# Performance work log

Measured on AMD Instinct MI355X. Metric: run time of the kernel, lower is better.

The kernel has to match this reference:

```python
import jax, jax.numpy as jnp
import numpy as np

B, T, D, U = 32, 4096, 512, 512

def setup_inputs() -> dict:
    key = jax.random.key(0)
    ks = jax.random.split(key, 8)
    s = 0.02
    return {
        "query": jax.random.normal(ks[0], (B, D), dtype=jnp.float32),
        "values": jax.random.normal(ks[1], (B, T, D), dtype=jnp.float32),
        "W1": jax.random.normal(ks[2], (D, U), dtype=jnp.float32) * s,
        "b1": jnp.zeros((U,), dtype=jnp.float32),
        "W2": jax.random.normal(ks[3], (D, U), dtype=jnp.float32) * s,
        "b2": jnp.zeros((U,), dtype=jnp.float32),
        "V": jax.random.normal(ks[4], (U, 1), dtype=jnp.float32) * s,
        "bv": jnp.zeros((1,), dtype=jnp.float32),
    }

def reference(query, values, W1, b1, W2, b2, V, bv):
    # query: [B, D] -> [B, 1, U]; values: [B, T, D] -> [B, T, U]
    q_proj = (query @ W1 + b1)[:, None, :]            # [B, 1, U]
    v_proj = values @ W2 + b2                          # [B, T, U]
    scores = jnp.tanh(q_proj + v_proj) @ V + bv        # [B, T, 1]
    attn = jax.nn.softmax(scores, axis=1)              # softmax over time axis
    context = jnp.sum(attn * values, axis=1)           # [B, D]
    return context
```

## Files before the change

### kernel.cpp

```cpp
#include <hip/hip_runtime.h>
#include <hip/hip_bf16.h>
#include <math.h>

#define B_ 32
#define T_ 4096
#define D_ 512
#define U_ 512

typedef __bf16 bf16x8 __attribute__((ext_vector_type(8)));
typedef float floatx4 __attribute__((ext_vector_type(4)));
typedef unsigned short ushortx8 __attribute__((ext_vector_type(8)));

static __device__ __forceinline__ unsigned short f2bf(float f) {
  unsigned int u = __float_as_uint(f);
  unsigned int r = (u + 0x7fffu + ((u >> 16) & 1u)) >> 16;
  return (unsigned short)r;
}

__global__ __launch_bounds__(256) void prep_w2t(
    const float* __restrict__ W2, unsigned short* __restrict__ W2T) {
  __shared__ float tile[32][33];
  const int bx = blockIdx.x * 32;
  const int by = blockIdx.y * 32;
  const int x = threadIdx.x;
#pragma unroll
  for (int y = threadIdx.y; y < 32; y += 8)
    tile[y][x] = W2[(size_t)(bx + y) * U_ + by + x];
  __syncthreads();
#pragma unroll
  for (int y = threadIdx.y; y < 32; y += 8)
    W2T[(size_t)(by + y) * D_ + bx + x] = f2bf(tile[x][y]);
}

__global__ __launch_bounds__(256) void qproj_kernel(
    const float* __restrict__ query, const float* __restrict__ W1,
    const float* __restrict__ b1, const float* __restrict__ b2,
    float* __restrict__ qp) {
  const int b = blockIdx.x;
  const int tid = threadIdx.x;
  __shared__ float qs[D_];
  qs[tid] = query[b * D_ + tid];
  qs[tid + 256] = query[b * D_ + tid + 256];
  __syncthreads();
  const int u0 = tid * 2;
  float ax = 0.f, ay = 0.f;
#pragma unroll 8
  for (int k = 0; k < D_; ++k) {
    const float q = qs[k];
    const float2 w = *(const float2*)&W1[(size_t)k * U_ + u0];
    ax += q * w.x;
    ay += q * w.y;
  }
  qp[b * U_ + u0] = ax + b1[u0] + b2[u0];
  qp[b * U_ + u0 + 1] = ay + b1[u0 + 1] + b2[u0 + 1];
}

__global__ __launch_bounds__(256) void scores_mfma(
    const float* __restrict__ values, const unsigned short* __restrict__ W2T,
    const float* __restrict__ qp, const float* __restrict__ V,
    float* __restrict__ scores) {
  const int b = blockIdx.y;
  const int t0 = blockIdx.x * 128;
  const int u0 = blockIdx.z * 128;
  const int tid = threadIdx.x;

  __shared__ __align__(16) unsigned short As[128 * 32];
  __shared__ __align__(16) unsigned short Bs[128 * 32];

  const int w = tid >> 6;
  const int lane = tid & 63;
  const int mo = (w & 1) * 64;
  const int no = (w >> 1) * 64;
  const int lr = lane & 15;
  const int koff = (lane >> 4) * 8;

  const float* vbase = values + ((size_t)b * T_ + t0) * D_;

  floatx4 acc[4][4];
#pragma unroll
  for (int i = 0; i < 4; ++i)
#pragma unroll
    for (int j = 0; j < 4; ++j) acc[i][j] = (floatx4)0.f;

  for (int k0 = 0; k0 < D_; k0 += 32) {
    __syncthreads();
#pragma unroll
    for (int p = 0; p < 2; ++p) {
      const int id = tid + 256 * p;
      const int r = id >> 2, c = (id & 3) * 8;
      const float4 f0 = *(const float4*)&vbase[(size_t)r * D_ + k0 + c];
      const float4 f1 = *(const float4*)&vbase[(size_t)r * D_ + k0 + c + 4];
      ushortx8 pk;
      pk[0] = f2bf(f0.x); pk[1] = f2bf(f0.y);
      pk[2] = f2bf(f0.z); pk[3] = f2bf(f0.w);
      pk[4] = f2bf(f1.x); pk[5] = f2bf(f1.y);
      pk[6] = f2bf(f1.z); pk[7] = f2bf(f1.w);
      *(ushortx8*)&As[r * 32 + c] = pk;
    }
#pragma unroll
    for (int p = 0; p < 2; ++p) {
      const int id = tid + 256 * p;
      const int r = id >> 2, c = (id & 3) * 8;
      *(ushortx8*)&Bs[r * 32 + c] =
          *(const ushortx8*)&W2T[(size_t)(u0 + r) * D_ + k0 + c];
    }
    __syncthreads();

    bf16x8 af[4], bf[4];
#pragma unroll
    for (int i = 0; i < 4; ++i)
      af[i] = __builtin_bit_cast(
          bf16x8, *(ushortx8*)&As[(mo + i * 16 + lr) * 32 + koff]);
#pragma unroll
    for (int j = 0; j < 4; ++j)
      bf[j] = __builtin_bit_cast(
          bf16x8, *(ushortx8*)&Bs[(no + j * 16 + lr) * 32 + koff]);
#pragma unroll
    for (int i = 0; i < 4; ++i)
#pragma unroll
      for (int j = 0; j < 4; ++j)
        acc[i][j] = __builtin_amdgcn_mfma_f32_16x16x32_bf16(af[i], bf[j],
                                                            acc[i][j], 0, 0, 0);
  }

  const float* qpb = qp + b * U_ + u0;
  float qv[4], vv[4];
#pragma unroll
  for (int j = 0; j < 4; ++j) {
    qv[j] = qpb[no + j * 16 + lr];
    vv[j] = V[u0 + no + j * 16 + lr];
  }
#pragma unroll
  for (int i = 0; i < 4; ++i) {
#pragma unroll
    for (int r = 0; r < 4; ++r) {
      float s = 0.f;
#pragma unroll
      for (int j = 0; j < 4; ++j) s += tanhf(acc[i][j][r] + qv[j]) * vv[j];
      s += __shfl_xor(s, 1);
      s += __shfl_xor(s, 2);
      s += __shfl_xor(s, 4);
      s += __shfl_xor(s, 8);
      if (lr == 0) {
        const int m = mo + i * 16 + (lane >> 4) * 4 + r;
        atomicAdd(&scores[(size_t)b * T_ + t0 + m], s);
      }
    }
  }
}

__global__ __launch_bounds__(256) void softmax_kernel(float* __restrict__ sc) {
  const int b = blockIdx.x;
  const int tid = threadIdx.x;
  __shared__ float red[256];
  float* s = sc + (size_t)b * T_;
  float v[16];
  float lmax = -1e30f;
#pragma unroll
  for (int i = 0; i < 16; ++i) {
    v[i] = s[tid + 256 * i];
    lmax = fmaxf(lmax, v[i]);
  }
  red[tid] = lmax;
  __syncthreads();
  for (int off = 128; off > 0; off >>= 1) {
    if (tid < off) red[tid] = fmaxf(red[tid], red[tid + off]);
    __syncthreads();
  }
  const float m = red[0];
  __syncthreads();
  float lsum = 0.f;
#pragma unroll
  for (int i = 0; i < 16; ++i) {
    v[i] = expf(v[i] - m);
    lsum += v[i];
  }
  red[tid] = lsum;
  __syncthreads();
  for (int off = 128; off > 0; off >>= 1) {
    if (tid < off) red[tid] += red[tid + off];
    __syncthreads();
  }
  const float inv = 1.0f / red[0];
#pragma unroll
  for (int i = 0; i < 16; ++i) s[tid + 256 * i] = v[i] * inv;
}

__global__ __launch_bounds__(256) void context_kernel(
    const float* __restrict__ values, const float* __restrict__ attn,
    float* __restrict__ out) {
  const int b = blockIdx.x;
  const int t0 = blockIdx.y * 128;
  const int tid = threadIdx.x;
  const int tx = tid & 127;
  const int ty = tid >> 7;
  __shared__ float as[128];
  __shared__ float4 red[128];
  if (tid < 128) as[tid] = attn[(size_t)b * T_ + t0 + tid];
  __syncthreads();
  const float* vb = values + ((size_t)b * T_ + t0) * D_;
  float ax = 0.f, ay = 0.f, az = 0.f, aw = 0.f;
#pragma unroll 4
  for (int t = ty; t < 128; t += 2) {
    const float a = as[t];
    const float4 v = *(const float4*)&vb[(size_t)t * D_ + tx * 4];
    ax += a * v.x;
    ay += a * v.y;
    az += a * v.z;
    aw += a * v.w;
  }
  if (ty == 1) red[tx] = make_float4(ax, ay, az, aw);
  __syncthreads();
  if (ty == 0) {
    const float4 o = red[tx];
    const int d = tx * 4;
    atomicAdd(&out[b * D_ + d],     ax + o.x);
    atomicAdd(&out[b * D_ + d + 1], ay + o.y);
    atomicAdd(&out[b * D_ + d + 2], az + o.z);
    atomicAdd(&out[b * D_ + d + 3], aw + o.w);
  }
}

extern "C" void kernel_launch(void* const* d_in, const int* in_sizes, int n_in,
                              void* d_out, int out_size, void* d_ws,
                              size_t ws_size, hipStream_t stream) {
  const float* query = (const float*)d_in[0];
  const float* values = (const float*)d_in[1];
  const float* W1 = (const float*)d_in[2];
  const float* b1 = (const float*)d_in[3];
  const float* W2 = (const float*)d_in[4];
  const float* b2 = (const float*)d_in[5];
  const float* V = (const float*)d_in[6];

  float* qp = (float*)d_ws;
  float* scores = qp + (size_t)B_ * U_;
  unsigned short* W2T = (unsigned short*)(scores + (size_t)B_ * T_);
  float* out = (float*)d_out;

  hipMemsetAsync(scores, 0, (size_t)B_ * T_ * sizeof(float), stream);
  hipMemsetAsync(d_out, 0, (size_t)B_ * D_ * sizeof(float), stream);

  prep_w2t<<<dim3(16, 16), dim3(32, 8), 0, stream>>>(W2, W2T);
  qproj_kernel<<<B_, 256, 0, stream>>>(query, W1, b1, b2, qp);
  scores_mfma<<<dim3(T_ / 128, B_, U_ / 128), 256, 0, stream>>>(values, W2T,
                                                                qp, V, scores);
  softmax_kernel<<<B_, 256, 0, stream>>>(scores);
  context_kernel<<<dim3(B_, 32), 256, 0, stream>>>(values, scores, out);
}
```

Before: 599.6 us.

## Give each scores block all U columns, stream W2 fragments from global, fast tanh

The scores kernel now tiles 64 time rows by the full 512 units per block, with each wave owning 128 units. The values tile is converted to bf16 once per row instead of once per U-tile, which cuts the fp32 values reads in the dominant GEMM fourfold. W2T fragments are loaded directly from global (L2-resident) instead of staged in LDS. The per-row partial sums are reduced in LDS and written with a plain store, which removes the atomics and the memset of scores. tanhf is replaced by an exp2/rcp approximation, and a context-loop unroll factor is raised. In exchange there are more accumulator registers per thread (occupancy hint of 2) and direct global B loads that may add latency.

```diff
diff --git a/kernel.cpp b/kernel.cpp
--- a/kernel.cpp
+++ b/kernel.cpp
@@ -15,6 +15,11 @@
   unsigned int u = __float_as_uint(f);
   unsigned int r = (u + 0x7fffu + ((u >> 16) & 1u)) >> 16;
   return (unsigned short)r;
+}
+
+static __device__ __forceinline__ float tanh_fast(float x) {
+  float e = exp2f(x * 2.88539008178f);
+  return 1.0f - 2.0f * __builtin_amdgcn_rcpf(1.0f + e);
 }
 
 __global__ __launch_bounds__(256) void prep_w2t(
@@ -55,98 +60,95 @@
   qp[b * U_ + u0 + 1] = ay + b1[u0 + 1] + b2[u0 + 1];
 }
 
-__global__ __launch_bounds__(256) void scores_mfma(
+__global__ __launch_bounds__(256, 2) void scores_mfma(
     const float* __restrict__ values, const unsigned short* __restrict__ W2T,
     const float* __restrict__ qp, const float* __restrict__ V,
     float* __restrict__ scores) {
   const int b = blockIdx.y;
-  const int t0 = blockIdx.x * 128;
-  const int u0 = blockIdx.z * 128;
-  const int tid = threadIdx.x;
-
-  __shared__ __align__(16) unsigned short As[128 * 32];
-  __shared__ __align__(16) unsigned short Bs[128 * 32];
-
+  const int t0 = blockIdx.x * 64;
+  const int tid = threadIdx.x;
   const int w = tid >> 6;
   const int lane = tid & 63;
-  const int mo = (w & 1) * 64;
-  const int no = (w >> 1) * 64;
   const int lr = lane & 15;
-  const int koff = (lane >> 4) * 8;
+  const int kc = lane >> 4;
+  const int no = w * 128;
+
+  __shared__ __align__(16) unsigned short As[4 * 528];
+  __shared__ float red[4][64];
 
   const float* vbase = values + ((size_t)b * T_ + t0) * D_;
-
-  floatx4 acc[4][4];
+  const int arow = tid >> 2;
+  const int achk = tid & 3;
+
+  floatx4 acc[4][8];
 #pragma unroll
   for (int i = 0; i < 4; ++i)
 #pragma unroll
-    for (int j = 0; j < 4; ++j) acc[i][j] = (floatx4)0.f;
+    for (int j = 0; j < 8; ++j) acc[i][j] = (floatx4)0.f;
 
   for (int k0 = 0; k0 < D_; k0 += 32) {
     __syncthreads();
-#pragma unroll
-    for (int p = 0; p < 2; ++p) {
-      const int id = tid + 256 * p;
-      const int r = id >> 2, c = (id & 3) * 8;
-      const float4 f0 = *(const float4*)&vbase[(size_t)r * D_ + k0 + c];
-      const float4 f1 = *(const float4*)&vbase[(size_t)r * D_ + k0 + c + 4];
+    {
+      const float4* vp = (const float4*)&vbase[(size_t)arow * D_ + k0 + achk * 8];
+      const float4 f0 = vp[0];
+      const float4 f1 = vp[1];
       ushortx8 pk;
       pk[0] = f2bf(f0.x); pk[1] = f2bf(f0.y);
       pk[2] = f2bf(f0.z); pk[3] = f2bf(f0.w);
       pk[4] = f2bf(f1.x); pk[5] = f2bf(f1.y);
       pk[6] = f2bf(f1.z); pk[7] = f2bf(f1.w);
-      *(ushortx8*)&As[r * 32 + c] = pk;
+      *(ushortx8*)&As[achk * 528 + arow * 8] = pk;
     }
-#pragma unroll
-    for (int p = 0; p < 2; ++p) {
-      const int id = tid + 256 * p;
-      const int r = id >> 2, c = (id & 3) * 8;
-      *(ushortx8*)&Bs[r * 32 + c] =
-          *(const ushortx8*)&W2T[(size_t)(u0 + r) * D_ + k0 + c];
-    }
-    __syncthreads();
-
-    bf16x8 af[4], bf[4];
+    __syncthreads();
+
+    bf16x8 bfr[8];
+#pragma unroll
+    for (int j = 0; j < 8; ++j)
+      bfr[j] = __builtin_bit_cast(
+          bf16x8,
+          *(const ushortx8*)&W2T[(size_t)(no + j * 16 + lr) * D_ + k0 + kc * 8]);
+
+    bf16x8 af[4];
 #pragma unroll
     for (int i = 0; i < 4; ++i)
       af[i] = __builtin_bit_cast(
-          bf16x8, *(ushortx8*)&As[(mo + i * 16 + lr) * 32 + koff]);
-#pragma unroll
-    for (int j = 0; j < 4; ++j)
-      bf[j] = __builtin_bit_cast(
-          bf16x8, *(ushortx8*)&Bs[(no + j * 16 + lr) * 32 + koff]);
+          bf16x8, *(ushortx8*)&As[kc * 528 + (i * 16 + lr) * 8]);
+
 #pragma unroll
     for (int i = 0; i < 4; ++i)
 #pragma unroll
-      for (int j = 0; j < 4; ++j)
-        acc[i][j] = __builtin_amdgcn_mfma_f32_16x16x32_bf16(af[i], bf[j],
+      for (int j = 0; j < 8; ++j)
+        acc[i][j] = __builtin_amdgcn_mfma_f32_16x16x32_bf16(af[i], bfr[j],
                                                             acc[i][j], 0, 0, 0);
   }
 
-  const float* qpb = qp + b * U_ + u0;
-  float qv[4], vv[4];
-#pragma unroll
-  for (int j = 0; j < 4; ++j) {
-    qv[j] = qpb[no + j * 16 + lr];
-    vv[j] = V[u0 + no + j * 16 + lr];
-  }
+  const float* qpb = qp + b * U_;
+  float qv[8], vv[8];
+#pragma unroll
+  for (int j = 0; j < 8; ++j) {
+    const int u = no + j * 16 + lr;
+    qv[j] = qpb[u];
+    vv[j] = V[u];
+  }
+  const int mrow = (lane >> 4) * 4;
 #pragma unroll
   for (int i = 0; i < 4; ++i) {
 #pragma unroll
     for (int r = 0; r < 4; ++r) {
       float s = 0.f;
 #pragma unroll
-      for (int j = 0; j < 4; ++j) s += tanhf(acc[i][j][r] + qv[j]) * vv[j];
+      for (int j = 0; j < 8; ++j) s += tanh_fast(acc[i][j][r] + qv[j]) * vv[j];
       s += __shfl_xor(s, 1);
       s += __shfl_xor(s, 2);
       s += __shfl_xor(s, 4);
       s += __shfl_xor(s, 8);
-      if (lr == 0) {
-        const int m = mo + i * 16 + (lane >> 4) * 4 + r;
-        atomicAdd(&scores[(size_t)b * T_ + t0 + m], s);
-      }
+      if (lr == 0) red[w][i * 16 + mrow + r] = s;
     }
   }
+  __syncthreads();
+  if (tid < 64)
+    scores[(size_t)b * T_ + t0 + tid] =
+        red[0][tid] + red[1][tid] + red[2][tid] + red[3][tid];
 }
 
 __global__ __launch_bounds__(256) void softmax_kernel(float* __restrict__ sc) {
@@ -200,7 +202,7 @@
   __syncthreads();
   const float* vb = values + ((size_t)b * T_ + t0) * D_;
   float ax = 0.f, ay = 0.f, az = 0.f, aw = 0.f;
-#pragma unroll 4
+#pragma unroll 8
   for (int t = ty; t < 128; t += 2) {
     const float a = as[t];
     const float4 v = *(const float4*)&vb[(size_t)t * D_ + tx * 4];
@@ -237,13 +239,12 @@
   unsigned short* W2T = (unsigned short*)(scores + (size_t)B_ * T_);
   float* out = (float*)d_out;
 
-  hipMemsetAsync(scores, 0, (size_t)B_ * T_ * sizeof(float), stream);
   hipMemsetAsync(d_out, 0, (size_t)B_ * D_ * sizeof(float), stream);
 
   prep_w2t<<<dim3(16, 16), dim3(32, 8), 0, stream>>>(W2, W2T);
   qproj_kernel<<<B_, 256, 0, stream>>>(query, W1, b1, b2, qp);
-  scores_mfma<<<dim3(T_ / 128, B_, U_ / 128), 256, 0, stream>>>(values, W2T,
-                                                                qp, V, scores);
+  scores_mfma<<<dim3(T_ / 64, B_), 256, 0, stream>>>(values, W2T, qp, V,
+                                                     scores);
   softmax_kernel<<<B_, 256, 0, stream>>>(scores);
   context_kernel<<<dim3(B_, 32), 256, 0, stream>>>(values, scores, out);
 }
```

After: 567.7 us. -5.3%, faster.
